# Optimization experiments

Measured on AMD Instinct MI355X. Metric: run time of the kernel, lower is better.

Reference implementation:

```python
import jax, jax.numpy as jnp
import numpy as np

B, S, D, H, HD = 2, 4096, 1024, 16, 64   # batch, seq, hidden, heads, head_dim
BLOCK, W = 64, 8                          # block size, local window in blocks (512 tokens)
ROPE_BASE = 10000.0


def _rope_tables(seq_len, dim, dtype):
    inv_freq = 1.0 / (ROPE_BASE ** (jnp.arange(0, dim, 2, dtype=jnp.float32) / dim))
    t = jnp.arange(seq_len, dtype=jnp.float32)
    freqs = jnp.einsum('i,j->ij', t, inv_freq)          # [S, dim/2]
    emb = jnp.concatenate([freqs, freqs], axis=-1)       # [S, dim]
    return jnp.cos(emb).astype(dtype), jnp.sin(emb).astype(dtype)


def _rotate_half(x):
    x1, x2 = x[..., : x.shape[-1] // 2], x[..., x.shape[-1] // 2:]
    return jnp.concatenate([-x2, x1], axis=-1)


def _apply_rope(q, k, position_ids):
    # q, k: [B, H, S, HD]; position_ids: [B, S]
    cos_t, sin_t = _rope_tables(S, HD, q.dtype)
    cos = cos_t[position_ids][:, None, :, :]             # [B, 1, S, HD]
    sin = sin_t[position_ids][:, None, :, :]
    q_emb = q * cos + _rotate_half(q) * sin
    k_emb = k * cos + _rotate_half(k) * sin
    return q_emb, k_emb


def _block_sparse_attention(q, k, v):
    # Causal block-sparse (sliding window of W blocks), DeepSpeed-style layout.
    # q, k, v: [B, H, S, HD]
    nb = S // BLOCK
    scale = 1.0 / jnp.sqrt(jnp.asarray(HD, q.dtype))
    qb = q.reshape(B, H, nb, BLOCK, HD)
    kb = k.reshape(B, H, nb, BLOCK, HD)
    vb = v.reshape(B, H, nb, BLOCK, HD)
    # block-column indices attended by each block-row: i-W+1 .. i
    idx = jnp.arange(nb)[:, None] - jnp.arange(W - 1, -1, -1)[None, :]   # [nb, W]
    valid = idx >= 0
    idxc = jnp.clip(idx, 0, nb - 1)
    kg = kb[:, :, idxc]                                   # [B, H, nb, W, BLOCK, HD]
    vg = vb[:, :, idxc]
    scores = jnp.einsum('bhnqd,bhnwkd->bhnqwk', qb, kg) * scale  # [B,H,nb,BLOCK,W,BLOCK]
    # absolute positions for causal mask within the window
    qpos = (jnp.arange(nb) * BLOCK)[:, None, None, None] + jnp.arange(BLOCK)[None, :, None, None]  # [nb,BLOCK,1,1]
    kpos = (idxc * BLOCK)[:, None, :, None] + jnp.arange(BLOCK)[None, None, None, :]               # [nb,1,W,BLOCK]
    mask = (kpos <= qpos) & valid[:, None, :, None]       # [nb, BLOCK, W, BLOCK]
    neg = jnp.asarray(-1e9, scores.dtype)
    scores = jnp.where(mask[None, None], scores, neg)
    scores = scores.reshape(B, H, nb, BLOCK, W * BLOCK)
    probs = jax.nn.softmax(scores, axis=-1)
    out = jnp.einsum('bhnqk,bhnkd->bhnqd', probs, vg.reshape(B, H, nb, W * BLOCK, HD))
    return out.reshape(B, H, S, HD)


def setup_inputs() -> dict:
    key = jax.random.key(0)
    ks = jax.random.split(key, 5)
    hidden_states = jax.random.normal(ks[0], (B, S, D), dtype=jnp.float32)
    position_ids = jnp.tile(jnp.arange(S, dtype=jnp.int32)[None, :], (B, 1))
    w_init = lambda k: (jax.random.normal(k, (D, D), dtype=jnp.float32) * 0.02)
    return {
        'hidden_states': hidden_states,
        'position_ids': position_ids,
        'wq': w_init(ks[1]),  # stored [in, out]
        'wk': w_init(ks[2]),
        'wv': w_init(ks[3]),
        'wo': w_init(ks[4]),
    }


def reference(hidden_states, position_ids, wq, wk, wv, wo):
    q = jnp.einsum('bsd,de->bse', hidden_states, wq).reshape(B, S, H, HD).transpose(0, 2, 1, 3)
    k = jnp.einsum('bsd,de->bse', hidden_states, wk).reshape(B, S, H, HD).transpose(0, 2, 1, 3)
    v = jnp.einsum('bsd,de->bse', hidden_states, wv).reshape(B, S, H, HD).transpose(0, 2, 1, 3)
    q, k = _apply_rope(q, k, position_ids)
    attn = _block_sparse_attention(q, k, v)               # [B, H, S, HD]
    attn = attn.transpose(0, 2, 1, 3).reshape(B, S, D)
    return jnp.einsum('bsd,de->bse', attn, wo)
```

## Files before the change

### kernel.cpp

```cpp
#include <hip/hip_runtime.h>
#include <cstdint>
#include <cstddef>

#define B_ 2
#define S_ 4096
#define D_ 1024
#define H_ 16
#define HD_ 64
#define NB_ 64
#define W_ 8
#define M_ (B_*S_)

#define QSCALE 0.18033688011112042f
#define LOG2_10000_OVER_32 0.41524101186092034f

typedef __bf16 bf16_t;
typedef __bf16 bf16x8 __attribute__((ext_vector_type(8)));
typedef float f32x4 __attribute__((ext_vector_type(4)));

#define GLOAD_LDS16(gp, lp) \
  __builtin_amdgcn_global_load_lds((__attribute__((address_space(1))) void*)(gp), \
                                   (__attribute__((address_space(3))) void*)(lp), 16, 0, 0)

__global__ void cast_bf16_kernel(const float* __restrict__ x, bf16_t* __restrict__ y, int n4) {
  int i = blockIdx.x * 256 + threadIdx.x;
  if (i >= n4) return;
  float4 v = ((const float4*)x)[i];
  union { bf16_t b[4]; uint2 u; } cv;
  cv.b[0] = (bf16_t)v.x; cv.b[1] = (bf16_t)v.y; cv.b[2] = (bf16_t)v.z; cv.b[3] = (bf16_t)v.w;
  ((uint2*)y)[i] = cv.u;
}

__global__ void transpose_cast_kernel(const float* __restrict__ w0, const float* __restrict__ w1,
                                      const float* __restrict__ w2, const float* __restrict__ w3,
                                      bf16_t* __restrict__ out) {
  const float* w = (blockIdx.z == 0) ? w0 : (blockIdx.z == 1) ? w1 : (blockIdx.z == 2) ? w2 : w3;
  bf16_t* wt = out + (size_t)blockIdx.z * D_ * D_;
  __shared__ float tile[32][33];
  int x = blockIdx.x * 32 + threadIdx.x;
  int y0 = blockIdx.y * 32;
  for (int i = threadIdx.y; i < 32; i += 8)
    tile[i][threadIdx.x] = w[(size_t)(y0 + i) * D_ + x];
  __syncthreads();
  int x2 = blockIdx.y * 32 + threadIdx.x;
  int y2 = blockIdx.x * 32;
  for (int i = threadIdx.y; i < 32; i += 8)
    wt[(size_t)(y2 + i) * D_ + x2] = (bf16_t)tile[threadIdx.x][i];
}

__global__ __launch_bounds__(512, 2) void gemm_qkv256(const bf16_t* __restrict__ A,
                                                      const bf16_t* __restrict__ Bt,
                                                      bf16_t* __restrict__ qkv,
                                                      bf16_t* __restrict__ vt_out,
                                                      const int* __restrict__ pos_ids) {
  const int bid = blockIdx.x;
  const int sid = (bid & 7) * 48 + (bid >> 3);
  const int mb = sid / 12, nb = sid % 12;
  const int mbase = mb * 256, nbase = nb * 256;
  const int tid = threadIdx.x;
  const int wid = tid >> 6, lane = tid & 63;
  const int quad = lane >> 4, l16 = lane & 15;
  const int wr = wid >> 2, wc = wid & 3;

  __shared__ bf16_t lds[4 * 16384];

  const int srow = wid * 16 + (lane >> 2);
  const int schunk = (lane & 3) ^ ((lane >> 3) & 3);
  const bf16_t* gAb = A  + (size_t)(mbase + srow) * D_ + schunk * 8;
  const bf16_t* gBb = Bt + (size_t)(nbase + srow) * D_ + schunk * 8;
  const int quadx = (quad ^ ((l16 >> 1) & 3)) * 8;

#define LDSA(b) (lds + (b) * 16384)
#define LDSB(b) (lds + (b) * 16384 + 8192)
#define STAGE_A(kt) do { bf16_t* p_ = LDSA((kt) & 3) + wid * 512; \
    GLOAD_LDS16(gAb + (kt) * 32, p_); \
    GLOAD_LDS16(gAb + (size_t)128 * D_ + (kt) * 32, p_ + 4096); } while (0)
#define STAGE_B(kt) do { bf16_t* p_ = LDSB((kt) & 3) + wid * 512; \
    GLOAD_LDS16(gBb + (kt) * 32, p_); \
    GLOAD_LDS16(gBb + (size_t)128 * D_ + (kt) * 32, p_ + 4096); } while (0)
#define WAITV(n) asm volatile("s_waitcnt vmcnt(" #n ")" ::: "memory")
#define BAR() do { __builtin_amdgcn_s_barrier(); asm volatile("" ::: "memory"); } while (0)

  f32x4 acc[8][4];
#pragma unroll
  for (int m = 0; m < 8; ++m)
#pragma unroll
    for (int n = 0; n < 4; ++n) acc[m][n] = (f32x4){0.f, 0.f, 0.f, 0.f};

#define PHASE(kt, STG, WT) do { \
    const bf16_t* Ab_ = LDSA((kt) & 3); \
    const bf16_t* Bb_ = LDSB((kt) & 3); \
    bf16x8 af_[8], bf_[4]; \
    _Pragma("unroll") \
    for (int m = 0; m < 8; ++m) \
      af_[m] = *(const bf16x8*)&Ab_[(wr * 128 + m * 16 + l16) * 32 + quadx]; \
    _Pragma("unroll") \
    for (int n = 0; n < 4; ++n) \
      bf_[n] = *(const bf16x8*)&Bb_[(wc * 64 + n * 16 + l16) * 32 + quadx]; \
    STG; \
    __builtin_amdgcn_s_setprio(1); \
    _Pragma("unroll") \
    for (int m = 0; m < 8; ++m) \
      _Pragma("unroll") \
      for (int n = 0; n < 4; ++n) \
        acc[m][n] = __builtin_amdgcn_mfma_f32_16x16x32_bf16(af_[m], bf_[n], acc[m][n], 0, 0, 0); \
    __builtin_amdgcn_s_setprio(0); \
    WT; \
    BAR(); \
  } while (0)

  STAGE_A(0); STAGE_B(0); STAGE_A(1); STAGE_B(1); STAGE_A(2); STAGE_B(2);
  WAITV(8);
  BAR();

  for (int kt = 0; kt < 29; ++kt)
    PHASE(kt, ({ STAGE_A(kt + 3); STAGE_B(kt + 3); }), WAITV(8));
  PHASE(29, (void)0, WAITV(4));
  PHASE(30, (void)0, WAITV(0));
  PHASE(31, (void)0, (void)0);

  const int zsl = nb >> 2;
  if (zsl < 2) {
    bf16_t* Cp = qkv + (size_t)zsl * M_ * D_;
    const float qsc = (zsl == 0) ? QSCALE : 1.0f;
    float invf[2];
#pragma unroll
    for (int ni = 0; ni < 2; ++ni)
      invf[ni] = __builtin_exp2f(-(float)(ni * 16 + l16) * LOG2_10000_OVER_32);
    const int colb = (nb & 3) * 256 + wc * 64;
#pragma unroll
    for (int m = 0; m < 8; ++m) {
#pragma unroll
      for (int r = 0; r < 4; ++r) {
        int row = mbase + wr * 128 + m * 16 + quad * 4 + r;
        float fpos = (float)pos_ids[row];
#pragma unroll
        for (int ni = 0; ni < 2; ++ni) {
          float sn, cs;
          __sincosf(fpos * invf[ni], &sn, &cs);
          float x1 = acc[m][ni][r], x2 = acc[m][ni + 2][r];
          int col = colb + ni * 16 + l16;
          Cp[(size_t)row * D_ + col]      = (bf16_t)((x1 * cs - x2 * sn) * qsc);
          Cp[(size_t)row * D_ + col + 32] = (bf16_t)((x2 * cs + x1 * sn) * qsc);
        }
      }
    }
  } else {
    const int h = (nb & 3) * 4 + wc;
#pragma unroll
    for (int mh = 0; mh < 2; ++mh) {
      int rowblk = mb * 4 + wr * 2 + mh;
      int bb = rowblk >> 6, sblk = rowblk & 63;
      size_t vbase = (size_t)(bb * H_ + h) * HD_ * S_;
#pragma unroll
      for (int n = 0; n < 4; ++n) {
        int d = n * 16 + l16;
        union { bf16_t bv[16]; uint4 u[2]; } pk;
#pragma unroll
        for (int r = 0; r < 4; ++r)
#pragma unroll
          for (int mi = 0; mi < 4; ++mi)
            pk.bv[r * 4 + mi] = (bf16_t)acc[mh * 4 + mi][n][r];
        size_t addr = vbase + (size_t)d * S_ + (size_t)sblk * 64 + quad * 16;
        *(uint4*)&vt_out[addr]     = pk.u[0];
        *(uint4*)&vt_out[addr + 8] = pk.u[1];
      }
    }
  }
#undef PHASE
#undef STAGE_A
#undef STAGE_B
#undef LDSA
#undef LDSB
#undef WAITV
#undef BAR
}

template<bool OBF>
__global__ __launch_bounds__(256) void gemm128(const bf16_t* __restrict__ A,
                                               const bf16_t* __restrict__ BtBase,
                                               void* __restrict__ Cbase,
                                               bf16_t* __restrict__ vt_out,
                                               const int* __restrict__ pos_ids) {
  const bf16_t* Bt = BtBase + (size_t)blockIdx.z * D_ * D_;
  const int mb = blockIdx.y * 128, nb = blockIdx.x * 128;
  const int tid = threadIdx.x;
  const int wid = tid >> 6, lane = tid & 63;
  const int quad = lane >> 4, l16 = lane & 15;
  const int wr = wid >> 1, wc = wid & 1;

  __shared__ bf16_t As[128 * 32];
  __shared__ bf16_t Bs[128 * 32];

  f32x4 acc[4][4];
#pragma unroll
  for (int mi = 0; mi < 4; ++mi)
#pragma unroll
    for (int ni = 0; ni < 4; ++ni)
      acc[mi][ni] = (f32x4){0.f, 0.f, 0.f, 0.f};

  const int acol = ((lane & 3) ^ ((lane >> 3) & 3)) * 8;
  const int arow0 = wid * 32 + (lane >> 2);
  const int quadx = (quad ^ ((l16 >> 1) & 3)) * 8;
  const bf16_t* gA = A + (size_t)(mb + arow0) * D_ + acol;
  const bf16_t* gB = Bt + (size_t)(nb + arow0) * D_ + acol;

  for (int kt = 0; kt < 32; ++kt) {
    const int k0 = kt * 32;
    __syncthreads();
#pragma unroll
    for (int c = 0; c < 2; ++c) {
      GLOAD_LDS16(gA + (size_t)c * 16 * D_ + k0, As + (wid * 2 + c) * 512);
      GLOAD_LDS16(gB + (size_t)c * 16 * D_ + k0, Bs + (wid * 2 + c) * 512);
    }
    __syncthreads();
    bf16x8 af[4], bfr[4];
#pragma unroll
    for (int mi = 0; mi < 4; ++mi)
      af[mi] = *(const bf16x8*)&As[(wr * 64 + mi * 16 + l16) * 32 + quadx];
#pragma unroll
    for (int ni = 0; ni < 4; ++ni)
      bfr[ni] = *(const bf16x8*)&Bs[(wc * 64 + ni * 16 + l16) * 32 + quadx];
#pragma unroll
    for (int mi = 0; mi < 4; ++mi)
#pragma unroll
      for (int ni = 0; ni < 4; ++ni)
        acc[mi][ni] = __builtin_amdgcn_mfma_f32_16x16x32_bf16(af[mi], bfr[ni], acc[mi][ni], 0, 0, 0);
  }

  if constexpr (OBF) {
  } else {
    float* Cp = (float*)Cbase;
#pragma unroll
    for (int mi = 0; mi < 4; ++mi)
#pragma unroll
      for (int ni = 0; ni < 4; ++ni)
#pragma unroll
        for (int r = 0; r < 4; ++r) {
          int row = mb + wr * 64 + mi * 16 + quad * 4 + r;
          int col = nb + wc * 64 + ni * 16 + l16;
          Cp[(size_t)row * D_ + col] = acc[mi][ni][r];
        }
  }
}

__global__ __launch_bounds__(256) void attn_kernel(const bf16_t* __restrict__ q,
                                                   const bf16_t* __restrict__ k,
                                                   const bf16_t* __restrict__ vt,
                                                   bf16_t* __restrict__ o) {
  const int m = blockIdx.x, h = blockIdx.y, b = blockIdx.z;
  const int n0 = m * 2, n1 = n0 + 1;
  const int tid = threadIdx.x;
  const int wid = tid >> 6, lane = tid & 63;
  const int quad = lane >> 4, l16 = lane & 15;

  __shared__ bf16_t Ks[64 * 72];
  __shared__ bf16_t Vs[64 * 72];
  __shared__ bf16_t Ps[4][16 * 72];

  const size_t hoff = (size_t)h * HD_;
  const size_t vtbase = (size_t)(b * H_ + h) * HD_ * S_;
  const size_t rowb[2] = {(size_t)(b * S_ + n0 * 64), (size_t)(b * S_ + n1 * 64)};

  bf16x8 aq[2][2];
#pragma unroll
  for (int x = 0; x < 2; ++x) {
    const bf16_t* qr = q + (rowb[x] + wid * 16 + l16) * D_ + hoff;
    aq[x][0] = *(const bf16x8*)(qr + quad * 8);
    aq[x][1] = *(const bf16x8*)(qr + 32 + quad * 8);
  }

  f32x4 o_acc[2][4];
  float lsum[2][4];
#pragma unroll
  for (int x = 0; x < 2; ++x)
#pragma unroll
    for (int t = 0; t < 4; ++t) {
      o_acc[x][t] = (f32x4){0.f, 0.f, 0.f, 0.f};
      lsum[x][t] = 0.f;
    }

  const int srow = tid >> 3;
  const int scol = (tid & 7) * 8;

  const int kb0 = (n0 >= W_ - 1) ? n0 - (W_ - 1) : 0;
  for (int kb = kb0; kb <= n1; ++kb) {
    __syncthreads();
    const size_t krow = (size_t)(b * S_ + kb * 64);
#pragma unroll
    for (int it = 0; it < 2; ++it) {
      int r = it * 32 + srow;
      *(uint4*)&Ks[r * 72 + scol] = *(const uint4*)&k[(krow + r) * D_ + hoff + scol];
      *(uint4*)&Vs[r * 72 + scol] = *(const uint4*)&vt[vtbase + (size_t)r * S_ + kb * 64 + scol];
    }
    __syncthreads();

#pragma unroll
    for (int x = 0; x < 2; ++x) {
      const int nx = n0 + x;
      if (x == 0 ? (kb > n0) : (kb < n1 - (W_ - 1))) continue;

      f32x4 sacc[4];
#pragma unroll
      for (int t = 0; t < 4; ++t) sacc[t] = (f32x4){0.f, 0.f, 0.f, 0.f};
#pragma unroll
      for (int t = 0; t < 4; ++t) {
        bf16x8 bk0 = *(const bf16x8*)&Ks[(t * 16 + l16) * 72 + quad * 8];
        bf16x8 bk1 = *(const bf16x8*)&Ks[(t * 16 + l16) * 72 + 32 + quad * 8];
        sacc[t] = __builtin_amdgcn_mfma_f32_16x16x32_bf16(aq[x][0], bk0, sacc[t], 0, 0, 0);
        sacc[t] = __builtin_amdgcn_mfma_f32_16x16x32_bf16(aq[x][1], bk1, sacc[t], 0, 0, 0);
      }

      const bool diag = (kb == nx);
#pragma unroll
      for (int r = 0; r < 4; ++r) {
        int qpos = wid * 16 + quad * 4 + r;
        union { bf16_t bv[4]; uint2 u; } pk;
        float rs = 0.f;
#pragma unroll
        for (int t = 0; t < 4; ++t) {
          float p = __builtin_exp2f(sacc[t][r]);
          if (diag && (t * 16 + l16 > qpos)) p = 0.f;
          rs += p;
          pk.bv[t] = (bf16_t)p;
        }
        lsum[x][r] += rs;
        *(uint2*)&Ps[wid][(quad * 4 + r) * 72 + l16 * 4] = pk.u;
      }

      bf16x8 pa0 = *(const bf16x8*)&Ps[wid][l16 * 72 + quad * 8];
      bf16x8 pa1 = *(const bf16x8*)&Ps[wid][l16 * 72 + 32 + quad * 8];
#pragma unroll
      for (int t = 0; t < 4; ++t) {
        bf16x8 vb0 = *(const bf16x8*)&Vs[(t * 16 + l16) * 72 + quad * 8];
        bf16x8 vb1 = *(const bf16x8*)&Vs[(t * 16 + l16) * 72 + 32 + quad * 8];
        o_acc[x][t] = __builtin_amdgcn_mfma_f32_16x16x32_bf16(pa0, vb0, o_acc[x][t], 0, 0, 0);
        o_acc[x][t] = __builtin_amdgcn_mfma_f32_16x16x32_bf16(pa1, vb1, o_acc[x][t], 0, 0, 0);
      }
    }
  }

#pragma unroll
  for (int x = 0; x < 2; ++x) {
    float inv[4];
#pragma unroll
    for (int r = 0; r < 4; ++r) {
      float s = lsum[x][r];
#pragma unroll
      for (int off = 1; off < 16; off <<= 1) s += __shfl_xor(s, off);
      inv[r] = 1.f / s;
    }
#pragma unroll
    for (int t = 0; t < 4; ++t)
#pragma unroll
      for (int r = 0; r < 4; ++r) {
        int row = wid * 16 + quad * 4 + r;
        int col = t * 16 + l16;
        o[(rowb[x] + row) * D_ + hoff + col] = (bf16_t)(o_acc[x][t][r] * inv[r]);
      }
  }
}

extern "C" void kernel_launch(void* const* d_in, const int* in_sizes, int n_in,
                              void* d_out, int out_size, void* d_ws, size_t ws_size,
                              hipStream_t stream) {
  const float* hs = (const float*)d_in[0];
  const int* pos  = (const int*)d_in[1];
  const float* wq = (const float*)d_in[2];
  const float* wk = (const float*)d_in[3];
  const float* wv = (const float*)d_in[4];
  const float* wo = (const float*)d_in[5];

  bf16_t* ws   = (bf16_t*)d_ws;
  bf16_t* hsb  = ws;
  bf16_t* wT   = hsb + (size_t)M_ * D_;
  bf16_t* qkv  = wT + (size_t)4 * D_ * D_;
  bf16_t* attn = qkv + (size_t)3 * M_ * D_;
  bf16_t* qw  = qkv;
  bf16_t* kw  = qkv + (size_t)M_ * D_;
  bf16_t* vtg = qkv + (size_t)2 * M_ * D_;

  cast_bf16_kernel<<<(M_ * D_ / 4 + 255) / 256, 256, 0, stream>>>(hs, hsb, M_ * D_ / 4);
  transpose_cast_kernel<<<dim3(D_ / 32, D_ / 32, 4), dim3(32, 8), 0, stream>>>(wq, wk, wv, wo, wT);
  gemm_qkv256<<<dim3(384), dim3(512), 0, stream>>>(hsb, wT, qkv, vtg, pos);
  attn_kernel<<<dim3(NB_ / 2, H_, B_), 256, 0, stream>>>(qw, kw, vtg, attn);
  gemm128<false><<<dim3(D_ / 128, M_ / 128, 1), 256, 0, stream>>>(attn, wT + (size_t)3 * D_ * D_, d_out, nullptr, pos);
}
```

Before: 243.0 us.

## Split GEMM k-phase into two half-tile MFMA phases and double-buffer attention K/V

The QKV GEMM main loop now splits each k-step into two phases that each load half the A fragments and run half the MFMAs. Global-to-LDS staging of A and B is spread across the two phases, with explicit barriers and lgkmcnt waits, which cuts register pressure and interleaves loads with compute. The attention kernel replaces synchronous global-to-register-to-LDS copies of K and V with double-buffered direct global_load_lds prefetch of the next key block, using an XOR-swizzled unpadded layout to avoid bank conflicts. The cost is extra barriers per k-step in the GEMM and added LDS for the second K/V buffer.

Result: no change. 243.0 us (+0.0%).

```diff
diff --git a/kernel.cpp b/kernel.cpp
--- a/kernel.cpp
+++ b/kernel.cpp
@@ -21,6 +21,8 @@
 #define GLOAD_LDS16(gp, lp) \
   __builtin_amdgcn_global_load_lds((__attribute__((address_space(1))) void*)(gp), \
                                    (__attribute__((address_space(3))) void*)(lp), 16, 0, 0)
+#define WAITV(n) asm volatile("s_waitcnt vmcnt(" #n ")" ::: "memory")
+#define BAR() do { __builtin_amdgcn_s_barrier(); asm volatile("" ::: "memory"); } while (0)
 
 __global__ void cast_bf16_kernel(const float* __restrict__ x, bf16_t* __restrict__ y, int n4) {
   int i = blockIdx.x * 256 + threadIdx.x;
@@ -78,8 +80,6 @@
 #define STAGE_B(kt) do { bf16_t* p_ = LDSB((kt) & 3) + wid * 512; \
     GLOAD_LDS16(gBb + (kt) * 32, p_); \
     GLOAD_LDS16(gBb + (size_t)128 * D_ + (kt) * 32, p_ + 4096); } while (0)
-#define WAITV(n) asm volatile("s_waitcnt vmcnt(" #n ")" ::: "memory")
-#define BAR() do { __builtin_amdgcn_s_barrier(); asm volatile("" ::: "memory"); } while (0)
 
   f32x4 acc[8][4];
 #pragma unroll
@@ -87,25 +87,47 @@
 #pragma unroll
     for (int n = 0; n < 4; ++n) acc[m][n] = (f32x4){0.f, 0.f, 0.f, 0.f};
 
-#define PHASE(kt, STG, WT) do { \
+  bf16x8 afr[4], bfr[4];
+
+#define PHASE0(kt, STG) do { \
     const bf16_t* Ab_ = LDSA((kt) & 3); \
     const bf16_t* Bb_ = LDSB((kt) & 3); \
-    bf16x8 af_[8], bf_[4]; \
     _Pragma("unroll") \
-    for (int m = 0; m < 8; ++m) \
-      af_[m] = *(const bf16x8*)&Ab_[(wr * 128 + m * 16 + l16) * 32 + quadx]; \
+    for (int mm = 0; mm < 4; ++mm) \
+      afr[mm] = *(const bf16x8*)&Ab_[(wr * 128 + mm * 16 + l16) * 32 + quadx]; \
     _Pragma("unroll") \
-    for (int n = 0; n < 4; ++n) \
-      bf_[n] = *(const bf16x8*)&Bb_[(wc * 64 + n * 16 + l16) * 32 + quadx]; \
+    for (int nn = 0; nn < 4; ++nn) \
+      bfr[nn] = *(const bf16x8*)&Bb_[(wc * 64 + nn * 16 + l16) * 32 + quadx]; \
     STG; \
+    BAR(); \
+    asm volatile("s_waitcnt lgkmcnt(0)" ::: "memory"); \
+    __builtin_amdgcn_sched_barrier(0); \
     __builtin_amdgcn_s_setprio(1); \
     _Pragma("unroll") \
-    for (int m = 0; m < 8; ++m) \
+    for (int mm = 0; mm < 4; ++mm) \
       _Pragma("unroll") \
-      for (int n = 0; n < 4; ++n) \
-        acc[m][n] = __builtin_amdgcn_mfma_f32_16x16x32_bf16(af_[m], bf_[n], acc[m][n], 0, 0, 0); \
+      for (int nn = 0; nn < 4; ++nn) \
+        acc[mm][nn] = __builtin_amdgcn_mfma_f32_16x16x32_bf16(afr[mm], bfr[nn], acc[mm][nn], 0, 0, 0); \
     __builtin_amdgcn_s_setprio(0); \
-    WT; \
+    BAR(); \
+  } while (0)
+
+#define PHASE1(kt, STG, WT) do { \
+    const bf16_t* Ab_ = LDSA((kt) & 3); \
+    _Pragma("unroll") \
+    for (int mm = 0; mm < 4; ++mm) \
+      afr[mm] = *(const bf16x8*)&Ab_[(wr * 128 + 64 + mm * 16 + l16) * 32 + quadx]; \
+    STG; WT; \
+    BAR(); \
+    asm volatile("s_waitcnt lgkmcnt(0)" ::: "memory"); \
+    __builtin_amdgcn_sched_barrier(0); \
+    __builtin_amdgcn_s_setprio(1); \
+    _Pragma("unroll") \
+    for (int mm = 0; mm < 4; ++mm) \
+      _Pragma("unroll") \
+      for (int nn = 0; nn < 4; ++nn) \
+        acc[4 + mm][nn] = __builtin_amdgcn_mfma_f32_16x16x32_bf16(afr[mm], bfr[nn], acc[4 + mm][nn], 0, 0, 0); \
+    __builtin_amdgcn_s_setprio(0); \
     BAR(); \
   } while (0)
 
@@ -113,11 +135,13 @@
   WAITV(8);
   BAR();
 
-  for (int kt = 0; kt < 29; ++kt)
-    PHASE(kt, ({ STAGE_A(kt + 3); STAGE_B(kt + 3); }), WAITV(8));
-  PHASE(29, (void)0, WAITV(4));
-  PHASE(30, (void)0, WAITV(0));
-  PHASE(31, (void)0, (void)0);
+  for (int kt = 0; kt < 29; ++kt) {
+    PHASE0(kt, STAGE_A(kt + 3));
+    PHASE1(kt, STAGE_B(kt + 3), WAITV(8));
+  }
+  PHASE0(29, (void)0); PHASE1(29, (void)0, WAITV(4));
+  PHASE0(30, (void)0); PHASE1(30, (void)0, WAITV(0));
+  PHASE0(31, (void)0); PHASE1(31, (void)0, (void)0);
 
   const int zsl = nb >> 2;
   if (zsl < 2) {
@@ -167,13 +191,12 @@
       }
     }
   }
-#undef PHASE
+#undef PHASE0
+#undef PHASE1
 #undef STAGE_A
 #undef STAGE_B
 #undef LDSA
 #undef LDSB
-#undef WAITV
-#undef BAR
 }
 
 template<bool OBF>
@@ -254,8 +277,8 @@
   const int wid = tid >> 6, lane = tid & 63;
   const int quad = lane >> 4, l16 = lane & 15;
 
-  __shared__ bf16_t Ks[64 * 72];
-  __shared__ bf16_t Vs[64 * 72];
+  __shared__ bf16_t Ks[2][64 * 64];
+  __shared__ bf16_t Vs[2][64 * 64];
   __shared__ bf16_t Ps[4][16 * 72];
 
   const size_t hoff = (size_t)h * HD_;
@@ -280,20 +303,31 @@
       lsum[x][t] = 0.f;
     }
 
-  const int srow = tid >> 3;
-  const int scol = (tid & 7) * 8;
+  const int srK = wid * 16 + (lane >> 3);
+  const int scC = ((lane & 7) ^ ((lane >> 3) & 7)) * 8;
+  const bf16_t* kbase = k + (size_t)(b * S_) * D_ + hoff;
+  const bf16_t* vbase2 = vt + vtbase;
+#define STAGE_KV(kb_, buf_) do { \
+    bf16_t* kd = &Ks[buf_][wid * 1024]; \
+    bf16_t* vd = &Vs[buf_][wid * 1024]; \
+    GLOAD_LDS16(kbase + (size_t)((kb_) * 64 + srK) * D_ + scC, kd); \
+    GLOAD_LDS16(kbase + (size_t)((kb_) * 64 + srK + 8) * D_ + scC, kd + 512); \
+    GLOAD_LDS16(vbase2 + (size_t)srK * S_ + (kb_) * 64 + scC, vd); \
+    GLOAD_LDS16(vbase2 + (size_t)(srK + 8) * S_ + (kb_) * 64 + scC, vd + 512); \
+  } while (0)
+
+  const int ck0 = (quad ^ (l16 & 7)) * 8;
+  const int ck1 = ((quad ^ 4) ^ (l16 & 7)) * 8;
 
   const int kb0 = (n0 >= W_ - 1) ? n0 - (W_ - 1) : 0;
+
+  STAGE_KV(kb0, kb0 & 1);
+
   for (int kb = kb0; kb <= n1; ++kb) {
-    __syncthreads();
-    const size_t krow = (size_t)(b * S_ + kb * 64);
-#pragma unroll
-    for (int it = 0; it < 2; ++it) {
-      int r = it * 32 + srow;
-      *(uint4*)&Ks[r * 72 + scol] = *(const uint4*)&k[(krow + r) * D_ + hoff + scol];
-      *(uint4*)&Vs[r * 72 + scol] = *(const uint4*)&vt[vtbase + (size_t)r * S_ + kb * 64 + scol];
-    }
-    __syncthreads();
+    const int buf = kb & 1;
+    if (kb < n1) { STAGE_KV(kb + 1, buf ^ 1); WAITV(4); }
+    else        { WAITV(0); }
+    BAR();
 
 #pragma unroll
     for (int x = 0; x < 2; ++x) {
@@ -305,8 +339,9 @@
       for (int t = 0; t < 4; ++t) sacc[t] = (f32x4){0.f, 0.f, 0.f, 0.f};
 #pragma unroll
       for (int t = 0; t < 4; ++t) {
-        bf16x8 bk0 = *(const bf16x8*)&Ks[(t * 16 + l16) * 72 + quad * 8];
-        bf16x8 bk1 = *(const bf16x8*)&Ks[(t * 16 + l16) * 72 + 32 + quad * 8];
+        const int rr = (t * 16 + l16) * 64;
+        bf16x8 bk0 = *(const bf16x8*)&Ks[buf][rr + ck0];
+        bf16x8 bk1 = *(const bf16x8*)&Ks[buf][rr + ck1];
         sacc[t] = __builtin_amdgcn_mfma_f32_16x16x32_bf16(aq[x][0], bk0, sacc[t], 0, 0, 0);
         sacc[t] = __builtin_amdgcn_mfma_f32_16x16x32_bf16(aq[x][1], bk1, sacc[t], 0, 0, 0);
       }
@@ -332,13 +367,16 @@
       bf16x8 pa1 = *(const bf16x8*)&Ps[wid][l16 * 72 + 32 + quad * 8];
 #pragma unroll
       for (int t = 0; t < 4; ++t) {
-        bf16x8 vb0 = *(const bf16x8*)&Vs[(t * 16 + l16) * 72 + quad * 8];
-        bf16x8 vb1 = *(const bf16x8*)&Vs[(t * 16 + l16) * 72 + 32 + quad * 8];
+        const int rr = (t * 16 + l16) * 64;
+        bf16x8 vb0 = *(const bf16x8*)&Vs[buf][rr + ck0];
+        bf16x8 vb1 = *(const bf16x8*)&Vs[buf][rr + ck1];
         o_acc[x][t] = __builtin_amdgcn_mfma_f32_16x16x32_bf16(pa0, vb0, o_acc[x][t], 0, 0, 0);
         o_acc[x][t] = __builtin_amdgcn_mfma_f32_16x16x32_bf16(pa1, vb1, o_acc[x][t], 0, 0, 0);
       }
     }
-  }
+    BAR();
+  }
+#undef STAGE_KV
 
 #pragma unroll
   for (int x = 0; x < 2; ++x) {
```

## Double-buffer attention K/V via async LDS loads; shrink QKV GEMM pipeline to three stages

Applied to the files above, without the earlier changes.

The attention kernel now stages K and V tiles into double-buffered LDS with global_load_lds and an XOR-swizzled layout, prefetching the next key block while computing the current one. This replaces the synchronous register-staged loads and their two barriers per step. The QKV GEMM drops from a 4-stage to a 3-stage LDS ring to cut LDS use, and its launch bounds ask for 4 blocks per SM. That larger occupancy request may force register spilling given the 8x4 accumulator tile.

Result: faster. 236.7 us (-2.6%).

```diff
diff --git a/kernel.cpp b/kernel.cpp
--- a/kernel.cpp
+++ b/kernel.cpp
@@ -21,6 +21,8 @@
 #define GLOAD_LDS16(gp, lp) \
   __builtin_amdgcn_global_load_lds((__attribute__((address_space(1))) void*)(gp), \
                                    (__attribute__((address_space(3))) void*)(lp), 16, 0, 0)
+#define WAITV(n) asm volatile("s_waitcnt vmcnt(" #n ")" ::: "memory")
+#define BAR() do { __builtin_amdgcn_s_barrier(); asm volatile("" ::: "memory"); } while (0)
 
 __global__ void cast_bf16_kernel(const float* __restrict__ x, bf16_t* __restrict__ y, int n4) {
   int i = blockIdx.x * 256 + threadIdx.x;
@@ -48,7 +50,7 @@
     wt[(size_t)(y2 + i) * D_ + x2] = (bf16_t)tile[threadIdx.x][i];
 }
 
-__global__ __launch_bounds__(512, 2) void gemm_qkv256(const bf16_t* __restrict__ A,
+__global__ __launch_bounds__(512, 4) void gemm_qkv256(const bf16_t* __restrict__ A,
                                                       const bf16_t* __restrict__ Bt,
                                                       bf16_t* __restrict__ qkv,
                                                       bf16_t* __restrict__ vt_out,
@@ -62,7 +64,7 @@
   const int quad = lane >> 4, l16 = lane & 15;
   const int wr = wid >> 2, wc = wid & 3;
 
-  __shared__ bf16_t lds[4 * 16384];
+  __shared__ bf16_t lds[3 * 16384];
 
   const int srow = wid * 16 + (lane >> 2);
   const int schunk = (lane & 3) ^ ((lane >> 3) & 3);
@@ -72,14 +74,12 @@
 
 #define LDSA(b) (lds + (b) * 16384)
 #define LDSB(b) (lds + (b) * 16384 + 8192)
-#define STAGE_A(kt) do { bf16_t* p_ = LDSA((kt) & 3) + wid * 512; \
-    GLOAD_LDS16(gAb + (kt) * 32, p_); \
-    GLOAD_LDS16(gAb + (size_t)128 * D_ + (kt) * 32, p_ + 4096); } while (0)
-#define STAGE_B(kt) do { bf16_t* p_ = LDSB((kt) & 3) + wid * 512; \
-    GLOAD_LDS16(gBb + (kt) * 32, p_); \
-    GLOAD_LDS16(gBb + (size_t)128 * D_ + (kt) * 32, p_ + 4096); } while (0)
-#define WAITV(n) asm volatile("s_waitcnt vmcnt(" #n ")" ::: "memory")
-#define BAR() do { __builtin_amdgcn_s_barrier(); asm volatile("" ::: "memory"); } while (0)
+#define STAGE(kt) do { bf16_t* pa_ = LDSA((kt) % 3) + wid * 512; \
+    bf16_t* pb_ = LDSB((kt) % 3) + wid * 512; \
+    GLOAD_LDS16(gAb + (kt) * 32, pa_); \
+    GLOAD_LDS16(gAb + (size_t)128 * D_ + (kt) * 32, pa_ + 4096); \
+    GLOAD_LDS16(gBb + (kt) * 32, pb_); \
+    GLOAD_LDS16(gBb + (size_t)128 * D_ + (kt) * 32, pb_ + 4096); } while (0)
 
   f32x4 acc[8][4];
 #pragma unroll
@@ -88,8 +88,8 @@
     for (int n = 0; n < 4; ++n) acc[m][n] = (f32x4){0.f, 0.f, 0.f, 0.f};
 
 #define PHASE(kt, STG, WT) do { \
-    const bf16_t* Ab_ = LDSA((kt) & 3); \
-    const bf16_t* Bb_ = LDSB((kt) & 3); \
+    const bf16_t* Ab_ = LDSA((kt) % 3); \
+    const bf16_t* Bb_ = LDSB((kt) % 3); \
     bf16x8 af_[8], bf_[4]; \
     _Pragma("unroll") \
     for (int m = 0; m < 8; ++m) \
@@ -109,13 +109,13 @@
     BAR(); \
   } while (0)
 
-  STAGE_A(0); STAGE_B(0); STAGE_A(1); STAGE_B(1); STAGE_A(2); STAGE_B(2);
-  WAITV(8);
+  STAGE(0); STAGE(1);
+  WAITV(4);
   BAR();
 
-  for (int kt = 0; kt < 29; ++kt)
-    PHASE(kt, ({ STAGE_A(kt + 3); STAGE_B(kt + 3); }), WAITV(8));
-  PHASE(29, (void)0, WAITV(4));
+#pragma unroll 3
+  for (int kt = 0; kt < 30; ++kt)
+    PHASE(kt, STAGE(kt + 2), WAITV(4));
   PHASE(30, (void)0, WAITV(0));
   PHASE(31, (void)0, (void)0);
 
@@ -168,12 +168,9 @@
     }
   }
 #undef PHASE
-#undef STAGE_A
-#undef STAGE_B
+#undef STAGE
 #undef LDSA
 #undef LDSB
-#undef WAITV
-#undef BAR
 }
 
 template<bool OBF>
@@ -254,8 +251,8 @@
   const int wid = tid >> 6, lane = tid & 63;
   const int quad = lane >> 4, l16 = lane & 15;
 
-  __shared__ bf16_t Ks[64 * 72];
-  __shared__ bf16_t Vs[64 * 72];
+  __shared__ bf16_t Ks[2][64 * 64];
+  __shared__ bf16_t Vs[2][64 * 64];
   __shared__ bf16_t Ps[4][16 * 72];
 
   const size_t hoff = (size_t)h * HD_;
@@ -280,20 +277,31 @@
       lsum[x][t] = 0.f;
     }
 
-  const int srow = tid >> 3;
-  const int scol = (tid & 7) * 8;
+  const int srK = wid * 16 + (lane >> 3);
+  const int scC = ((lane & 7) ^ ((lane >> 3) & 7)) * 8;
+  const bf16_t* kbase = k + (size_t)(b * S_) * D_ + hoff;
+  const bf16_t* vbase2 = vt + vtbase;
+#define STAGE_KV(kb_, buf_) do { \
+    bf16_t* kd = &Ks[buf_][wid * 1024]; \
+    bf16_t* vd = &Vs[buf_][wid * 1024]; \
+    GLOAD_LDS16(kbase + (size_t)((kb_) * 64 + srK) * D_ + scC, kd); \
+    GLOAD_LDS16(kbase + (size_t)((kb_) * 64 + srK + 8) * D_ + scC, kd + 512); \
+    GLOAD_LDS16(vbase2 + (size_t)srK * S_ + (kb_) * 64 + scC, vd); \
+    GLOAD_LDS16(vbase2 + (size_t)(srK + 8) * S_ + (kb_) * 64 + scC, vd + 512); \
+  } while (0)
+
+  const int ck0 = (quad ^ (l16 & 7)) * 8;
+  const int ck1 = ((quad ^ 4) ^ (l16 & 7)) * 8;
 
   const int kb0 = (n0 >= W_ - 1) ? n0 - (W_ - 1) : 0;
+
+  STAGE_KV(kb0, kb0 & 1);
+
   for (int kb = kb0; kb <= n1; ++kb) {
-    __syncthreads();
-    const size_t krow = (size_t)(b * S_ + kb * 64);
-#pragma unroll
-    for (int it = 0; it < 2; ++it) {
-      int r = it * 32 + srow;
-      *(uint4*)&Ks[r * 72 + scol] = *(const uint4*)&k[(krow + r) * D_ + hoff + scol];
-      *(uint4*)&Vs[r * 72 + scol] = *(const uint4*)&vt[vtbase + (size_t)r * S_ + kb * 64 + scol];
-    }
-    __syncthreads();
+    const int buf = kb & 1;
+    if (kb < n1) { STAGE_KV(kb + 1, buf ^ 1); WAITV(4); }
+    else        { WAITV(0); }
+    BAR();
 
 #pragma unroll
     for (int x = 0; x < 2; ++x) {
@@ -305,8 +313,9 @@
       for (int t = 0; t < 4; ++t) sacc[t] = (f32x4){0.f, 0.f, 0.f, 0.f};
 #pragma unroll
       for (int t = 0; t < 4; ++t) {
-        bf16x8 bk0 = *(const bf16x8*)&Ks[(t * 16 + l16) * 72 + quad * 8];
-        bf16x8 bk1 = *(const bf16x8*)&Ks[(t * 16 + l16) * 72 + 32 + quad * 8];
+        const int rr = (t * 16 + l16) * 64;
+        bf16x8 bk0 = *(const bf16x8*)&Ks[buf][rr + ck0];
+        bf16x8 bk1 = *(const bf16x8*)&Ks[buf][rr + ck1];
         sacc[t] = __builtin_amdgcn_mfma_f32_16x16x32_bf16(aq[x][0], bk0, sacc[t], 0, 0, 0);
         sacc[t] = __builtin_amdgcn_mfma_f32_16x16x32_bf16(aq[x][1], bk1, sacc[t], 0, 0, 0);
       }
@@ -332,13 +341,16 @@
       bf16x8 pa1 = *(const bf16x8*)&Ps[wid][l16 * 72 + 32 + quad * 8];
 #pragma unroll
       for (int t = 0; t < 4; ++t) {
-        bf16x8 vb0 = *(const bf16x8*)&Vs[(t * 16 + l16) * 72 + quad * 8];
-        bf16x8 vb1 = *(const bf16x8*)&Vs[(t * 16 + l16) * 72 + 32 + quad * 8];
+        const int rr = (t * 16 + l16) * 64;
+        bf16x8 vb0 = *(const bf16x8*)&Vs[buf][rr + ck0];
+        bf16x8 vb1 = *(const bf16x8*)&Vs[buf][rr + ck1];
         o_acc[x][t] = __builtin_amdgcn_mfma_f32_16x16x32_bf16(pa0, vb0, o_acc[x][t], 0, 0, 0);
         o_acc[x][t] = __builtin_amdgcn_mfma_f32_16x16x32_bf16(pa1, vb1, o_acc[x][t], 0, 0, 0);
       }
     }
-  }
+    BAR();
+  }
+#undef STAGE_KV
 
 #pragma unroll
   for (int x = 0; x < 2; ++x) {
```
